# Kernel tuning notes

Measured on AMD Instinct MI355X. Metric: run time of the kernel, lower is better.

## Reference

```python
import jax, jax.numpy as jnp
import numpy as np

N_IN = 1024
N_OUT = 2048
EMBED_DIM = 1024  # == n_in so multi-layer path type-checks
LAYERS = 2
T, B = 128, 64


def setup_inputs() -> dict:
    key = jax.random.key(0)
    ks = jax.random.split(key, 8)
    s_in = 1.0 / np.sqrt(N_IN)
    s_out = 1.0 / np.sqrt(N_OUT)
    return {
        "xt": jax.random.normal(ks[0], (T, B, N_IN), jnp.float32),
        "ct_forward": jnp.zeros((LAYERS, B, N_OUT), jnp.float32),
        # weights stored [in, out] (transposed vs torch Linear)
        "Wx": jax.random.uniform(ks[1], (N_IN, N_OUT), jnp.float32, -s_in, s_in),
        "Wf": jax.random.uniform(ks[2], (N_IN, N_OUT), jnp.float32, -s_in, s_in),
        "bf": jnp.zeros((N_OUT,), jnp.float32),
        "Wr": jax.random.uniform(ks[3], (N_IN, N_OUT), jnp.float32, -s_in, s_in),
        "br": jnp.zeros((N_OUT,), jnp.float32),
        "Wcx": jax.random.uniform(ks[4], (N_IN, N_OUT), jnp.float32, -s_in, s_in),
        "bcx": jnp.zeros((N_OUT,), jnp.float32),
        "Wcl": jax.random.uniform(ks[5], (N_OUT, EMBED_DIM), jnp.float32, -s_out, s_out),
        "bcl": jnp.zeros((EMBED_DIM,), jnp.float32),
    }


def _one_layer(x, c0, Wx, Wf, bf, Wr, br, Wcx, bcx):
    # x: [T, B, n_in]; c0: [B, n_out]
    # batch all projections over time (compute-dense GEMMs)
    xp = jnp.einsum("tbi,io->tbo", x, Wx)                     # x_t projection
    f = jax.nn.sigmoid(jnp.einsum("tbi,io->tbo", x, Wf) + bf)  # forget gate
    r = jax.nn.sigmoid(jnp.einsum("tbi,io->tbo", x, Wr) + br)  # reset gate
    cx = jnp.einsum("tbi,io->tbo", x, Wcx) + bcx               # highway path

    def step(c, inp):
        f_t, xp_t = inp
        c_new = f_t * c + (1.0 - f_t) * xp_t
        return c_new, c_new

    c_last, c_seq = jax.lax.scan(step, c0, (f, xp))
    h = r * jnp.tanh(c_seq) + (1.0 - r) * cx
    return h, c_last


def reference(xt, ct_forward, Wx, Wf, bf, Wr, br, Wcx, bcx, Wcl, bcl):
    x = xt
    c_last = ct_forward[0]
    for l in range(LAYERS):
        if x.shape[2] == N_OUT:  # layers >= 2: project back to embed_dim (= n_in)
            x = jnp.einsum("tbo,oe->tbe", x, Wcl) + bcl
        x, c_last = _one_layer(x, ct_forward[l], Wx, Wf, bf, Wr, br, Wcx, bcx)
    # dropout p=0.0 -> identity
    return x, c_last
```

## Files before the change

### kernel.cpp

```cpp
#include <hip/hip_runtime.h>

#define TT 128
#define BB 64
#define NIN 1024
#define NOUT 2048
#define MR (TT*BB)

typedef unsigned short u16;
typedef __attribute__((ext_vector_type(8))) __bf16 bf16x8;
typedef __attribute__((ext_vector_type(4))) float f32x4;
typedef __attribute__((ext_vector_type(8))) unsigned short u16x8;

static __device__ __forceinline__ u16 f2bf(float f) {
    union { float f; unsigned u; } v; v.f = f;
    unsigned r = v.u + 0x7fffu + ((v.u >> 16) & 1u);
    return (u16)(r >> 16);
}
static __device__ __forceinline__ float bf2f(u16 x) {
    union { unsigned u; float f; } v; v.u = ((unsigned)x) << 16;
    return v.f;
}

__global__ void k_cvt_chunk(const float* __restrict__ s, u16* __restrict__ d, int M_, int K_) {
    __shared__ float t[64][33];
    int m0 = blockIdx.x * 64, k0 = blockIdx.y * 32;
    int ml = threadIdx.x >> 3, kl = (threadIdx.x & 7) * 4;
    #pragma unroll
    for (int p = 0; p < 2; ++p) {
        float4 v = *(const float4*)&s[(size_t)(m0 + ml + p * 32) * K_ + k0 + kl];
        t[ml + p * 32][kl] = v.x; t[ml + p * 32][kl + 1] = v.y;
        t[ml + p * 32][kl + 2] = v.z; t[ml + p * 32][kl + 3] = v.w;
    }
    __syncthreads();
    int q = threadIdx.x >> 6, row = threadIdx.x & 63;
    u16x8 o;
    #pragma unroll
    for (int j = 0; j < 8; ++j) o[j] = f2bf(t[row][q * 8 + j]);
    *(u16x8*)&d[(((size_t)(k0 >> 3) + q) * M_ + m0 + row) * 8] = o;
}

__global__ void k_wT_chunk(const float* __restrict__ s, u16* __restrict__ d,
                           int K_, int N_, int OUTM, int row_off) {
    __shared__ float t[32][65];
    int k0 = blockIdx.y * 32, n0 = blockIdx.x * 64;
    int kl = threadIdx.x >> 6, nl = threadIdx.x & 63;
    #pragma unroll
    for (int p = 0; p < 8; ++p)
        t[kl + p * 4][nl] = s[(size_t)(k0 + kl + p * 4) * N_ + n0 + nl];
    __syncthreads();
    int q = threadIdx.x >> 6, row = threadIdx.x & 63;
    u16x8 o;
    #pragma unroll
    for (int j = 0; j < 8; ++j) o[j] = f2bf(t[q * 8 + j][row]);
    *(u16x8*)&d[(((size_t)(k0 >> 3) + q) * OUTM + row_off + n0 + row) * 8] = o;
}

__global__ void k_bias_pack(const float* __restrict__ bf_, const float* __restrict__ br_,
                            const float* __restrict__ bcx_, float* __restrict__ ball) {
    int i = blockIdx.x * 256 + threadIdx.x;
    int g = i >> 11, n = i & 2047;
    float v = 0.f;
    if (g == 1) v = bf_[n];
    else if (g == 2) v = br_[n];
    else if (g == 3) v = bcx_[n];
    ball[i] = v;
}

#define GLL16(SRC, DST) __builtin_amdgcn_global_load_lds( \
    (const __attribute__((address_space(1))) void*)(SRC), \
    (__attribute__((address_space(3))) void*)(DST), 16, 0, 0)
#define SBAR() __builtin_amdgcn_s_barrier()
#define SCHED0() __builtin_amdgcn_sched_barrier(0)

__global__ __launch_bounds__(512, 2) void k_gemm8(
    const u16* __restrict__ A, const u16* __restrict__ BT,
    const float* __restrict__ bias, u16* __restrict__ outG,
    int M, int NB, int K)
{
    constexpr int BM = 256;
    constexpr int BUF = BM * 32 + 8192;
    __shared__ __align__(16) u16 L[4 * BUF];

    const int tid = threadIdx.x;
    const int w = tid >> 6, lane = tid & 63;
    const int wr = w >> 2, wc = w & 3;
    const int lr = lane & 15, kq = lane >> 4;
    const int gx = gridDim.x;
    const int nwg = gx * gridDim.y;
    const int flat = blockIdx.y * gx + blockIdx.x;
    const int swz = (flat & 7) * (nwg >> 3) + (flat >> 3);
    const int m0 = (swz / gx) * BM, n0 = (swz % gx) * 256;
    const int nk = K >> 5;

    const u16* aSrc[2]; int aDst[2];
    #pragma unroll
    for (int l = 0; l < 2; ++l) {
        int tc = tid + l * 512;
        aSrc[l] = A + ((size_t)(tc >> 8) * M + m0 + (tc & 255)) * 8;
        aDst[l] = (w * 64 + l * 512) * 8;
    }
    const u16* bSrc[2]; int bDst[2];
    #pragma unroll
    for (int l = 0; l < 2; ++l) {
        int tc = tid + l * 512;
        bSrc[l] = BT + ((size_t)(tc >> 8) * NB + n0 + (tc & 255)) * 8;
        bDst[l] = BM * 32 + (w * 64 + l * 512) * 8;
    }
    const size_t aStep = (size_t)32 * M;
    const size_t bStep = (size_t)32 * NB;
    const int rdA = wr * 128 + lr;
    const int rdB = wc * 64 + lr;

    f32x4 acc[8][4] = {};
    bf16x8 aP0[4], bP0[4], aP1[4], bP1[4];

    #pragma unroll
    for (int p = 0; p < 3; ++p) {
        #pragma unroll
        for (int l = 0; l < 2; ++l) GLL16(aSrc[l] + (size_t)p * aStep, &L[p * BUF + aDst[l]]);
        #pragma unroll
        for (int l = 0; l < 2; ++l) GLL16(bSrc[l] + (size_t)p * bStep, &L[p * BUF + bDst[l]]);
    }
    asm volatile("s_waitcnt vmcnt(4)" ::: "memory");
    SBAR(); SCHED0();
    #pragma unroll
    for (int i = 0; i < 4; ++i) aP0[i] = *(const bf16x8*)&L[(kq * BM + rdA + i * 16) * 8];
    #pragma unroll
    for (int j = 0; j < 4; ++j) bP0[j] = *(const bf16x8*)&L[BM * 32 + (kq * 256 + rdB + j * 16) * 8];

#define ITER8(KT, CUR, NXT) { \
    const int kt_ = (KT); \
    const int bb = (kt_ & 3) * BUF; \
    const int tn = (kt_ + 1 < nk) ? kt_ + 1 : nk - 1; \
    const int nb = (tn & 3) * BUF; \
    bf16x8 aG[4]; \
    _Pragma("unroll") for (int i = 0; i < 4; ++i) \
        aG[i] = *(const bf16x8*)&L[bb + (kq * BM + rdA + 64 + i * 16) * 8]; \
    if (kt_ + 3 < nk) { \
        const size_t sa = (size_t)(kt_ + 3) * aStep, sb_ = (size_t)(kt_ + 3) * bStep; \
        const int wb = ((kt_ + 3) & 3) * BUF; \
        _Pragma("unroll") for (int l = 0; l < 2; ++l) GLL16(aSrc[l] + sa, &L[wb + aDst[l]]); \
        _Pragma("unroll") for (int l = 0; l < 2; ++l) GLL16(bSrc[l] + sb_, &L[wb + bDst[l]]); \
    } \
    __builtin_amdgcn_s_setprio(1); \
    _Pragma("unroll") for (int i = 0; i < 4; ++i) \
        _Pragma("unroll") for (int j = 0; j < 4; ++j) \
            acc[i][j] = __builtin_amdgcn_mfma_f32_16x16x32_bf16(aP##CUR[i], bP##CUR[j], acc[i][j], 0, 0, 0); \
    _Pragma("unroll") for (int i = 0; i < 4; ++i) \
        aP##NXT[i] = *(const bf16x8*)&L[nb + (kq * BM + rdA + i * 16) * 8]; \
    _Pragma("unroll") for (int j = 0; j < 4; ++j) \
        bP##NXT[j] = *(const bf16x8*)&L[nb + BM * 32 + (kq * 256 + rdB + j * 16) * 8]; \
    _Pragma("unroll") for (int i = 0; i < 4; ++i) \
        _Pragma("unroll") for (int j = 0; j < 4; ++j) \
            acc[i + 4][j] = __builtin_amdgcn_mfma_f32_16x16x32_bf16(aG[i], bP##CUR[j], acc[i + 4][j], 0, 0, 0); \
    __builtin_amdgcn_s_setprio(0); \
    asm volatile("s_waitcnt vmcnt(4)" ::: "memory"); \
    SBAR(); SCHED0(); }

    for (int kt4 = 0; kt4 < nk; kt4 += 4) {
        ITER8(kt4 + 0, 0, 1);
        ITER8(kt4 + 1, 1, 0);
        ITER8(kt4 + 2, 0, 1);
        ITER8(kt4 + 3, 1, 0);
    }
#undef ITER8

    const size_t GM2 = (size_t)M << 11;
    #pragma unroll
    for (int i = 0; i < 8; ++i) {
        int r0 = m0 + wr * 128 + i * 16 + kq * 4;
        #pragma unroll
        for (int j = 0; j < 4; ++j) {
            int gc = n0 + wc * 64 + j * 16 + lr;
            float bv = bias[gc];
            int g = gc >> 11;
            bool sig = (g == 1 || g == 2);
            size_t base = (size_t)g * GM2 + (size_t)(gc & 2047);
            #pragma unroll
            for (int q = 0; q < 4; ++q) {
                float v = acc[i][j][q] + bv;
                if (sig) v = 1.f / (1.f + __expf(-v));
                outG[base + (size_t)(r0 + q) * 2048] = f2bf(v);
            }
        }
    }
}

__global__ __launch_bounds__(512, 2) void k_gemm4(
    const u16* __restrict__ A, const u16* __restrict__ BT,
    const float* __restrict__ bias, u16* __restrict__ outC,
    int M, int NB, int K)
{
    constexpr int BM = 128;
    constexpr int BUF = BM * 32 + 8192;
    __shared__ __align__(16) u16 L[4 * BUF];

    const int tid = threadIdx.x;
    const int w = tid >> 6, lane = tid & 63;
    const int wr = w >> 2, wc = w & 3;
    const int lr = lane & 15, kq = lane >> 4;
    const int gx = gridDim.x;
    const int nwg = gx * gridDim.y;
    const int flat = blockIdx.y * gx + blockIdx.x;
    const int swz = (flat & 7) * (nwg >> 3) + (flat >> 3);
    const int m0 = (swz / gx) * BM, n0 = (swz % gx) * 256;
    const int nk = K >> 5;

    const u16* aSrc1; int aDst1;
    {
        int q = tid >> 7, row = tid & 127;
        aSrc1 = A + ((size_t)q * M + m0 + row) * 8;
        aDst1 = (w * 64) * 8;
    }
    const u16* bSrc[2]; int bDst[2];
    #pragma unroll
    for (int l = 0; l < 2; ++l) {
        int tc = tid + l * 512;
        bSrc[l] = BT + ((size_t)(tc >> 8) * NB + n0 + (tc & 255)) * 8;
        bDst[l] = BM * 32 + (w * 64 + l * 512) * 8;
    }
    const size_t aStep = (size_t)32 * M;
    const size_t bStep = (size_t)32 * NB;
    const int rdA = wr * 64 + lr;
    const int rdB = wc * 64 + lr;

    f32x4 acc[4][4] = {};
    bf16x8 aP0[4], bP0[4], aP1[4], bP1[4];

    #pragma unroll
    for (int p = 0; p < 3; ++p) {
        GLL16(aSrc1 + (size_t)p * aStep, &L[p * BUF + aDst1]);
        #pragma unroll
        for (int l = 0; l < 2; ++l) GLL16(bSrc[l] + (size_t)p * bStep, &L[p * BUF + bDst[l]]);
    }
    asm volatile("s_waitcnt vmcnt(3)" ::: "memory");
    SBAR(); SCHED0();
    #pragma unroll
    for (int i = 0; i < 4; ++i) aP0[i] = *(const bf16x8*)&L[(kq * BM + rdA + i * 16) * 8];
    #pragma unroll
    for (int j = 0; j < 4; ++j) bP0[j] = *(const bf16x8*)&L[BM * 32 + (kq * 256 + rdB + j * 16) * 8];

#define ITER4(KT, CUR, NXT) { \
    const int kt_ = (KT); \
    const int tn = (kt_ + 1 < nk) ? kt_ + 1 : nk - 1; \
    const int nb = (tn & 3) * BUF; \
    if (kt_ + 3 < nk) { \
        const size_t sa = (size_t)(kt_ + 3) * aStep, sb_ = (size_t)(kt_ + 3) * bStep; \
        const int wb = ((kt_ + 3) & 3) * BUF; \
        GLL16(aSrc1 + sa, &L[wb + aDst1]); \
        _Pragma("unroll") for (int l = 0; l < 2; ++l) GLL16(bSrc[l] + sb_, &L[wb + bDst[l]]); \
    } \
    __builtin_amdgcn_s_setprio(1); \
    _Pragma("unroll") for (int i = 0; i < 4; ++i) \
        _Pragma("unroll") for (int j = 0; j < 4; ++j) \
            acc[i][j] = __builtin_amdgcn_mfma_f32_16x16x32_bf16(aP##CUR[i], bP##CUR[j], acc[i][j], 0, 0, 0); \
    _Pragma("unroll") for (int i = 0; i < 4; ++i) \
        aP##NXT[i] = *(const bf16x8*)&L[nb + (kq * BM + rdA + i * 16) * 8]; \
    _Pragma("unroll") for (int j = 0; j < 4; ++j) \
        bP##NXT[j] = *(const bf16x8*)&L[nb + BM * 32 + (kq * 256 + rdB + j * 16) * 8]; \
    __builtin_amdgcn_s_setprio(0); \
    asm volatile("s_waitcnt vmcnt(3)" ::: "memory"); \
    SBAR(); SCHED0(); }

    for (int kt4 = 0; kt4 < nk; kt4 += 4) {
        ITER4(kt4 + 0, 0, 1);
        ITER4(kt4 + 1, 1, 0);
        ITER4(kt4 + 2, 0, 1);
        ITER4(kt4 + 3, 1, 0);
    }
#undef ITER4

    #pragma unroll
    for (int i = 0; i < 4; ++i) {
        int r0 = m0 + wr * 64 + i * 16 + kq * 4;
        #pragma unroll
        for (int j = 0; j < 4; ++j) {
            int gc = n0 + wc * 64 + j * 16 + lr;
            float bv = bias[gc];
            size_t base = ((size_t)(gc >> 3) * M) * 8 + (size_t)(gc & 7);
            #pragma unroll
            for (int q = 0; q < 4; ++q)
                outC[base + (size_t)(r0 + q) * 8] = f2bf(acc[i][j][q] + bv);
        }
    }
}

__global__ void k_scan(const u16* __restrict__ G, const float* __restrict__ c0,
                       u16* __restrict__ hb, float* __restrict__ hf,
                       float* __restrict__ cout)
{
    int idx = blockIdx.x * 256 + threadIdx.x;
    int b = idx >> 11, n = idx & 2047;
    float c = c0[idx];
    const size_t GM = (size_t)MR * 2048;
    const size_t hcBase = ((size_t)(n >> 3) * MR) * 8 + (size_t)(n & 7);
    for (int t = 0; t < TT; ++t) {
        int m = t * BB + b;
        size_t p = ((size_t)m << 11) + (size_t)n;
        float xp = bf2f(G[p]);
        float f  = bf2f(G[GM + p]);
        float r  = bf2f(G[2 * GM + p]);
        float cx = bf2f(G[3 * GM + p]);
        c = f * c + (1.f - f) * xp;
        float h = r * tanhf(c) + (1.f - r) * cx;
        if (hb) hb[hcBase + (size_t)m * 8] = f2bf(h);
        if (hf) hf[p] = h;
    }
    if (cout) cout[idx] = c;
}

extern "C" void kernel_launch(void* const* d_in, const int* in_sizes, int n_in,
                              void* d_out, int out_size, void* d_ws, size_t ws_size,
                              hipStream_t stream)
{
    const float* xt  = (const float*)d_in[0];
    const float* ctf = (const float*)d_in[1];
    const float* Wx  = (const float*)d_in[2];
    const float* Wf  = (const float*)d_in[3];
    const float* bfp = (const float*)d_in[4];
    const float* Wr  = (const float*)d_in[5];
    const float* brp = (const float*)d_in[6];
    const float* Wcx = (const float*)d_in[7];
    const float* bcx = (const float*)d_in[8];
    const float* Wcl = (const float*)d_in[9];
    const float* bcl = (const float*)d_in[10];
    float* out = (float*)d_out;

    char* ws = (char*)d_ws;
    u16* x0 = (u16*)ws;       ws += (size_t)MR * NIN * 2;
    u16* x2 = (u16*)ws;       ws += (size_t)MR * NIN * 2;
    u16* h1 = (u16*)ws;       ws += (size_t)MR * NOUT * 2;
    u16* WTall = (u16*)ws;    ws += (size_t)4 * NOUT * NIN * 2;
    u16* WclT = (u16*)ws;     ws += (size_t)NIN * NOUT * 2;
    float* ball = (float*)ws; ws += (size_t)4 * NOUT * 4;
    u16* G = (u16*)ws;        ws += (size_t)4 * MR * NOUT * 2;

    k_cvt_chunk<<<dim3(MR / 64, NIN / 32), 256, 0, stream>>>(xt, x0, MR, NIN);
    k_wT_chunk<<<dim3(NOUT / 64, NIN / 32), 256, 0, stream>>>(Wx,  WTall, NIN, NOUT, 4 * NOUT, 0 * NOUT);
    k_wT_chunk<<<dim3(NOUT / 64, NIN / 32), 256, 0, stream>>>(Wf,  WTall, NIN, NOUT, 4 * NOUT, 1 * NOUT);
    k_wT_chunk<<<dim3(NOUT / 64, NIN / 32), 256, 0, stream>>>(Wr,  WTall, NIN, NOUT, 4 * NOUT, 2 * NOUT);
    k_wT_chunk<<<dim3(NOUT / 64, NIN / 32), 256, 0, stream>>>(Wcx, WTall, NIN, NOUT, 4 * NOUT, 3 * NOUT);
    k_wT_chunk<<<dim3(NIN / 64, NOUT / 32), 256, 0, stream>>>(Wcl, WclT, NOUT, NIN, NIN, 0);
    k_bias_pack<<<32, 256, 0, stream>>>(bfp, brp, bcx, ball);

    k_gemm8<<<dim3(32, 32), 512, 0, stream>>>(x0, WTall, ball, G, MR, 4 * NOUT, NIN);
    k_scan<<<(BB * NOUT) / 256, 256, 0, stream>>>(G, ctf, h1, (float*)nullptr, (float*)nullptr);

    k_gemm4<<<dim3(NIN / 256, MR / 128), 512, 0, stream>>>(h1, WclT, bcl, x2, MR, NIN, NOUT);

    k_gemm8<<<dim3(32, 32), 512, 0, stream>>>(x2, WTall, ball, G, MR, 4 * NOUT, NIN);
    k_scan<<<(BB * NOUT) / 256, 256, 0, stream>>>(G, ctf + (size_t)BB * NOUT, (u16*)nullptr, out, out + (size_t)MR * NOUT);
}
```

Baseline: 470.2 us.

## Restructure GEMM main loop into double-buffered 64-K tiles with half-stage prefetch

Replaces the 4-buffer, 32-wide K pipeline with two 64-wide K buffers, each split into two 32-K halves that are staged asynchronously, with explicit barriers around MFMA groups and fewer fragment registers. It also changes the block-to-tile mapping so each XCD handles a contiguous group of N tiles. The aim is better overlap of global-to-LDS loads with MFMA and better L2 locality. In exchange it adds more barriers per K step, and the hand-counted vmcnt waits are fragile.

```diff
diff --git a/kernel.cpp b/kernel.cpp
--- a/kernel.cpp
+++ b/kernel.cpp
@@ -71,99 +71,84 @@
     (__attribute__((address_space(3))) void*)(DST), 16, 0, 0)
 #define SBAR() __builtin_amdgcn_s_barrier()
 #define SCHED0() __builtin_amdgcn_sched_barrier(0)
+#define VM8 asm volatile("s_waitcnt vmcnt(8)" ::: "memory")
+#define VM4 asm volatile("s_waitcnt vmcnt(4)" ::: "memory")
+#define VM0 asm volatile("s_waitcnt vmcnt(0)" ::: "memory")
 
 __global__ __launch_bounds__(512, 2) void k_gemm8(
     const u16* __restrict__ A, const u16* __restrict__ BT,
     const float* __restrict__ bias, u16* __restrict__ outG,
     int M, int NB, int K)
 {
-    constexpr int BM = 256;
-    constexpr int BUF = BM * 32 + 8192;
-    __shared__ __align__(16) u16 L[4 * BUF];
+    __shared__ __align__(16) u16 L[65536];
 
     const int tid = threadIdx.x;
     const int w = tid >> 6, lane = tid & 63;
     const int wr = w >> 2, wc = w & 3;
     const int lr = lane & 15, kq = lane >> 4;
-    const int gx = gridDim.x;
-    const int nwg = gx * gridDim.y;
-    const int flat = blockIdx.y * gx + blockIdx.x;
-    const int swz = (flat & 7) * (nwg >> 3) + (flat >> 3);
-    const int m0 = (swz / gx) * BM, n0 = (swz % gx) * 256;
-    const int nk = K >> 5;
-
-    const u16* aSrc[2]; int aDst[2];
-    #pragma unroll
-    for (int l = 0; l < 2; ++l) {
-        int tc = tid + l * 512;
-        aSrc[l] = A + ((size_t)(tc >> 8) * M + m0 + (tc & 255)) * 8;
-        aDst[l] = (w * 64 + l * 512) * 8;
-    }
-    const u16* bSrc[2]; int bDst[2];
-    #pragma unroll
-    for (int l = 0; l < 2; ++l) {
-        int tc = tid + l * 512;
-        bSrc[l] = BT + ((size_t)(tc >> 8) * NB + n0 + (tc & 255)) * 8;
-        bDst[l] = BM * 32 + (w * 64 + l * 512) * 8;
-    }
-    const size_t aStep = (size_t)32 * M;
-    const size_t bStep = (size_t)32 * NB;
-    const int rdA = wr * 128 + lr;
-    const int rdB = wc * 64 + lr;
+    const int flat = blockIdx.y * gridDim.x + blockIdx.x;
+    const int xcd = flat & 7, bi = flat >> 3;
+    const int n0 = (xcd * 4 + (bi & 3)) * 256;
+    const int m0 = (bi >> 2) * 256;
+    const int nk = K >> 6;
+
+    const int t1 = tid + 512;
+    const u16* aS0 = A + ((size_t)(tid >> 8) * M + m0 + (tid & 255)) * 8;
+    const u16* aS1 = A + ((size_t)(t1 >> 8) * M + m0 + (t1 & 255)) * 8;
+    const u16* bS0 = BT + ((size_t)(tid >> 8) * NB + n0 + (tid & 255)) * 8;
+    const u16* bS1 = BT + ((size_t)(t1 >> 8) * NB + n0 + (t1 & 255)) * 8;
+    const int aD0 = (w * 64) * 8, aD1 = (w * 64 + 512) * 8;
 
     f32x4 acc[8][4] = {};
-    bf16x8 aP0[4], bP0[4], aP1[4], bP1[4];
-
-    #pragma unroll
-    for (int p = 0; p < 3; ++p) {
-        #pragma unroll
-        for (int l = 0; l < 2; ++l) GLL16(aSrc[l] + (size_t)p * aStep, &L[p * BUF + aDst[l]]);
-        #pragma unroll
-        for (int l = 0; l < 2; ++l) GLL16(bSrc[l] + (size_t)p * bStep, &L[p * BUF + bDst[l]]);
-    }
-    asm volatile("s_waitcnt vmcnt(4)" ::: "memory");
-    SBAR(); SCHED0();
-    #pragma unroll
-    for (int i = 0; i < 4; ++i) aP0[i] = *(const bf16x8*)&L[(kq * BM + rdA + i * 16) * 8];
-    #pragma unroll
-    for (int j = 0; j < 4; ++j) bP0[j] = *(const bf16x8*)&L[BM * 32 + (kq * 256 + rdB + j * 16) * 8];
-
-#define ITER8(KT, CUR, NXT) { \
-    const int kt_ = (KT); \
-    const int bb = (kt_ & 3) * BUF; \
-    const int tn = (kt_ + 1 < nk) ? kt_ + 1 : nk - 1; \
-    const int nb = (tn & 3) * BUF; \
-    bf16x8 aG[4]; \
-    _Pragma("unroll") for (int i = 0; i < 4; ++i) \
-        aG[i] = *(const bf16x8*)&L[bb + (kq * BM + rdA + 64 + i * 16) * 8]; \
-    if (kt_ + 3 < nk) { \
-        const size_t sa = (size_t)(kt_ + 3) * aStep, sb_ = (size_t)(kt_ + 3) * bStep; \
-        const int wb = ((kt_ + 3) & 3) * BUF; \
-        _Pragma("unroll") for (int l = 0; l < 2; ++l) GLL16(aSrc[l] + sa, &L[wb + aDst[l]]); \
-        _Pragma("unroll") for (int l = 0; l < 2; ++l) GLL16(bSrc[l] + sb_, &L[wb + bDst[l]]); \
-    } \
-    __builtin_amdgcn_s_setprio(1); \
+
+#define STAGE(TAU, KH, BUFB) { \
+    const size_t oA = ((size_t)(TAU) * 8 + (KH) * 4) * (size_t)M * 8; \
+    const size_t oB = ((size_t)(TAU) * 8 + (KH) * 4) * (size_t)NB * 8; \
+    GLL16(aS0 + oA, &L[(BUFB) + (KH) * 8192 + aD0]); \
+    GLL16(aS1 + oA, &L[(BUFB) + (KH) * 8192 + aD1]); \
+    GLL16(bS0 + oB, &L[(BUFB) + 16384 + (KH) * 8192 + aD0]); \
+    GLL16(bS1 + oB, &L[(BUFB) + 16384 + (KH) * 8192 + aD1]); }
+
+#define LDA(BUFB, KH, RB) { _Pragma("unroll") for (int i = 0; i < 4; ++i) \
+    aF[i] = *(const bf16x8*)&L[(BUFB) + (KH) * 8192 + (kq * 256 + wr * 128 + (RB) * 64 + i * 16 + lr) * 8]; }
+#define LDB(BUFB, KH) { _Pragma("unroll") for (int j = 0; j < 4; ++j) \
+    bF[j] = *(const bf16x8*)&L[(BUFB) + 16384 + (KH) * 8192 + (kq * 256 + wc * 64 + j * 16 + lr) * 8]; }
+#define MM(RO) { __builtin_amdgcn_s_setprio(1); \
     _Pragma("unroll") for (int i = 0; i < 4; ++i) \
         _Pragma("unroll") for (int j = 0; j < 4; ++j) \
-            acc[i][j] = __builtin_amdgcn_mfma_f32_16x16x32_bf16(aP##CUR[i], bP##CUR[j], acc[i][j], 0, 0, 0); \
-    _Pragma("unroll") for (int i = 0; i < 4; ++i) \
-        aP##NXT[i] = *(const bf16x8*)&L[nb + (kq * BM + rdA + i * 16) * 8]; \
-    _Pragma("unroll") for (int j = 0; j < 4; ++j) \
-        bP##NXT[j] = *(const bf16x8*)&L[nb + BM * 32 + (kq * 256 + rdB + j * 16) * 8]; \
-    _Pragma("unroll") for (int i = 0; i < 4; ++i) \
-        _Pragma("unroll") for (int j = 0; j < 4; ++j) \
-            acc[i + 4][j] = __builtin_amdgcn_mfma_f32_16x16x32_bf16(aG[i], bP##CUR[j], acc[i + 4][j], 0, 0, 0); \
-    __builtin_amdgcn_s_setprio(0); \
-    asm volatile("s_waitcnt vmcnt(4)" ::: "memory"); \
-    SBAR(); SCHED0(); }
-
-    for (int kt4 = 0; kt4 < nk; kt4 += 4) {
-        ITER8(kt4 + 0, 0, 1);
-        ITER8(kt4 + 1, 1, 0);
-        ITER8(kt4 + 2, 0, 1);
-        ITER8(kt4 + 3, 1, 0);
-    }
-#undef ITER8
+            acc[(RO) + i][j] = __builtin_amdgcn_mfma_f32_16x16x32_bf16(aF[i], bF[j], acc[(RO) + i][j], 0, 0, 0); \
+    __builtin_amdgcn_s_setprio(0); }
+
+    STAGE(0, 0, 0); STAGE(0, 1, 0); STAGE(1, 0, 32768);
+    VM8; SBAR(); SCHED0();
+
+    for (int it = 0; it < nk / 2; ++it) {
+        const int t = 2 * it;
+        const bool st2 = (t + 2) < nk, st3 = (t + 3) < nk;
+        bf16x8 aF[4], bF[4];
+        LDA(0, 0, 0); LDB(0, 0); STAGE(t + 1, 1, 32768);
+        SBAR(); MM(0); SBAR();
+        LDA(0, 0, 1);
+        SBAR(); MM(4); VM8; SBAR(); SCHED0();
+        LDA(0, 1, 0); LDB(0, 1); if (st2) STAGE(t + 2, 0, 0);
+        SBAR(); MM(0); SBAR();
+        LDA(0, 1, 1);
+        SBAR(); MM(4); if (st2) { VM8; } else { VM4; } SBAR(); SCHED0();
+        LDA(32768, 0, 0); LDB(32768, 0); if (st2) STAGE(t + 2, 1, 0);
+        SBAR(); MM(0); SBAR();
+        LDA(32768, 0, 1);
+        SBAR(); MM(4); if (st2) { VM8; } else { VM0; } SBAR(); SCHED0();
+        LDA(32768, 1, 0); LDB(32768, 1); if (st3) STAGE(t + 3, 0, 32768);
+        SBAR(); MM(0); SBAR();
+        LDA(32768, 1, 1);
+        SBAR(); MM(4);
+        if (st2) { if (st3) { VM8; } else { VM4; } } else { VM0; }
+        SBAR(); SCHED0();
+    }
+#undef STAGE
+#undef LDA
+#undef LDB
+#undef MM
 
     const size_t GM2 = (size_t)M << 11;
     #pragma unroll
```

After: 486.3 us. 1.03x slower.
